# Optimization experiments

Measured on AMD Instinct MI355X. Metric: run time of the kernel, lower is better.

The kernel has to match this reference:

```python
import jax, jax.numpy as jnp
import numpy as np

N, E = 10000, 320000
F_N, F_E, F_G, LATENT, F_OUT = 128, 128, 32, 128, 128


def _make_mlp_params(key, dims):
    # dims: list of layer widths, e.g. [256,128,128,128,256]
    params = []
    for i in range(len(dims) - 1):
        key, k1, k2 = jax.random.split(key, 3)
        lim = 1.0 / np.sqrt(dims[i])
        w = jax.random.uniform(k1, (dims[i], dims[i + 1]), jnp.float32, -lim, lim)
        b = jax.random.uniform(k2, (dims[i + 1],), jnp.float32, -lim, lim)
        params.append((w, b))
    return params, key


def _mlp(h, ws, bs, activate_final):
    n = len(ws)
    for i in range(n):
        h = h @ ws[i] + bs[i]
        if i < n - 1 or activate_final:
            h = jax.nn.relu(h)
    return h


def setup_inputs() -> dict:
    key = jax.random.key(0)
    key, kx, ke, kg, ki = jax.random.split(key, 5)
    x = jax.random.normal(kx, (N, F_N), jnp.float32)
    edge_index = jax.random.randint(ki, (2, E), 0, N, jnp.int64)
    edge_attr = jax.random.normal(ke, (E, F_E), jnp.float32)
    global_attr = jax.random.normal(kg, (1, F_G), jnp.float32)

    # node_mlp_1: (F_N+F_E) -> L -> L -> L -> (F_N+F_E), activate_final=True
    p1, key = _make_mlp_params(key, [F_N + F_E, LATENT, LATENT, LATENT, F_N + F_E])
    # node_mlp_2: (2*F_N+F_E+F_G) -> L -> L -> L -> F_OUT, activate_final=False
    p2, key = _make_mlp_params(key, [2 * F_N + F_E + F_G, LATENT, LATENT, LATENT, F_OUT])

    inp = {"x": x, "edge_index": edge_index, "edge_attr": edge_attr, "global_attr": global_attr}
    for i, (w, b) in enumerate(p1):
        inp[f"m1_w{i}"] = w
        inp[f"m1_b{i}"] = b
    for i, (w, b) in enumerate(p2):
        inp[f"m2_w{i}"] = w
        inp[f"m2_b{i}"] = b
    return inp


def reference(x, edge_index, edge_attr, global_attr,
              m1_w0, m1_b0, m1_w1, m1_b1, m1_w2, m1_b2, m1_w3, m1_b3,
              m2_w0, m2_b0, m2_w1, m2_b1, m2_w2, m2_b2, m2_w3, m2_b3):
    row, col = edge_index[0], edge_index[1]
    n = x.shape[0]
    # gather sender-side node feats, per-edge MLP (activate_final=True)
    h = jnp.concatenate([x[row], edge_attr], axis=1)          # [E, F_N+F_E]
    h = _mlp(h, [m1_w0, m1_w1, m1_w2, m1_w3], [m1_b0, m1_b1, m1_b2, m1_b3], True)
    # scatter_mean over destination nodes
    s = jax.ops.segment_sum(h, col, num_segments=n)           # [N, F_N+F_E]
    cnt = jax.ops.segment_sum(jnp.ones((h.shape[0],), h.dtype), col, num_segments=n)
    agg = s / jnp.maximum(cnt, 1.0)[:, None]
    # repeat global feats to N rows (pad_to_size mode='repeat', G divides N)
    g = jnp.tile(global_attr, (n // global_attr.shape[0], 1))  # [N, F_G]
    out = jnp.concatenate([x, agg, g], axis=1)                 # [N, 2F_N+F_E+F_G]
    return _mlp(out, [m2_w0, m2_w1, m2_w2, m2_w3], [m2_b0, m2_b1, m2_b2, m2_b3], False)
```

## Files before the change

kernel.cpp:

```cpp
#include <hip/hip_runtime.h>

#define E_EDGES 320000
#define N_NODES 10000

typedef __attribute__((ext_vector_type(8))) short short8;
typedef __attribute__((ext_vector_type(4))) float floatx4;
typedef __attribute__((ext_vector_type(4))) short short4v;

__device__ __forceinline__ float bf2f(unsigned short u) {
    union { unsigned int i; float f; } v; v.i = ((unsigned int)u) << 16; return v.f;
}
__device__ __forceinline__ unsigned short f2bf(float f) {
    union { float f; unsigned int i; } v; v.f = f;
    unsigned int u = v.i;
    return (unsigned short)((u + 0x7fffu + ((u >> 16) & 1u)) >> 16);
}

template<int K, int Nn, int NT>
__device__ __forceinline__ void layer_acc(const unsigned short* __restrict__ in, int istride,
                                          const unsigned short* __restrict__ wt,
                                          int lane, int n0, floatx4 (&acc)[4][NT])
{
    const int quad = lane >> 4;
    const int mrow = lane & 15;
    floatx4 zero = {0.f, 0.f, 0.f, 0.f};
#pragma unroll
    for (int mt = 0; mt < 4; ++mt)
#pragma unroll
        for (int nt = 0; nt < NT; ++nt)
            acc[mt][nt] = zero;

#pragma unroll
    for (int kt = 0; kt < K / 32; ++kt) {
        const int koff = kt * 32 + quad * 8;
        short8 a[4];
        short8 b[NT];
#pragma unroll
        for (int mt = 0; mt < 4; ++mt)
            a[mt] = *(const short8*)&in[(mt * 16 + mrow) * istride + koff];
#pragma unroll
        for (int nt = 0; nt < NT; ++nt)
            b[nt] = *(const short8*)&wt[(size_t)(kt * (Nn >> 4) + (n0 >> 4) + nt) * 512 + lane * 8];
#pragma unroll
        for (int nt = 0; nt < NT; ++nt)
#pragma unroll
            for (int mt = 0; mt < 4; ++mt)
                acc[mt][nt] = __builtin_amdgcn_mfma_f32_16x16x32_bf16(a[mt], b[nt], acc[mt][nt], 0, 0, 0);
    }
}

template<int NT>
__device__ __forceinline__ void store_lds(floatx4 (&acc)[4][NT], const float* __restrict__ bias,
                                          int lane, int n0, unsigned short* __restrict__ out, int ostride,
                                          bool relu)
{
    const int quad = lane >> 4, mrow = lane & 15;
#pragma unroll
    for (int nt = 0; nt < NT; ++nt) {
        int col = n0 + nt * 16 + mrow;
        float bv = bias[col];
#pragma unroll
        for (int mt = 0; mt < 4; ++mt) {
#pragma unroll
            for (int r = 0; r < 4; ++r) {
                float v = acc[mt][nt][r] + bv;
                if (relu) v = v > 0.f ? v : 0.f;
                out[(mt * 16 + quad * 4 + r) * ostride + col] = f2bf(v);
            }
        }
    }
}

struct TDesc { const float* src; unsigned short* dst; int nElem; int logN; int blockStart; };
struct TArgs { TDesc d[8]; };

__global__ void transpose_kernel(TArgs a)
{
    int b = blockIdx.x;
    int i = 0;
#pragma unroll
    for (int j = 1; j < 8; ++j)
        if (b >= a.d[j].blockStart) i = j;
    const TDesc t = a.d[i];
    int idx = (b - t.blockStart) * 256 + threadIdx.x;
    if (idx < t.nElem) {
        int n = idx & ((1 << t.logN) - 1);
        int k = idx >> t.logN;
        int ntiles = 1 << (t.logN - 4);
        size_t dsti = ((size_t)(k >> 5) * ntiles + (n >> 4)) * 512
                    + ((k >> 3) & 3) * 128 + (n & 15) * 8 + (k & 7);
        t.dst[dsti] = f2bf(t.src[idx]);
    }
}

__global__ void hist_kernel(const int* __restrict__ eidx, int* __restrict__ cnt)
{
    int e = blockIdx.x * 256 + threadIdx.x;
    atomicAdd(&cnt[eidx[E_EDGES + e]], 1);
}

__global__ void scan_kernel(const int* __restrict__ cnt, int* __restrict__ fill)
{
    __shared__ int partial[256];
    const int CH = 40;
    int tid = threadIdx.x;
    int base = tid * CH;
    int local[CH];
    int sum = 0;
#pragma unroll
    for (int j = 0; j < CH; ++j) {
        int idx = base + j;
        int c = (idx < N_NODES) ? cnt[idx] : 0;
        local[j] = c;
        sum += c;
    }
    partial[tid] = sum;
    __syncthreads();
    for (int o = 1; o < 256; o <<= 1) {
        int v = (tid >= o) ? partial[tid - o] : 0;
        __syncthreads();
        partial[tid] += v;
        __syncthreads();
    }
    int run = partial[tid] - sum;
#pragma unroll
    for (int j = 0; j < CH; ++j) {
        int idx = base + j;
        if (idx < N_NODES) fill[idx] = run;
        run += local[j];
    }
}

__global__ void fill_kernel(const int* __restrict__ eidx, int* __restrict__ fill,
                            int* __restrict__ elist, int* __restrict__ rowp, int* __restrict__ dstp)
{
    int e = blockIdx.x * 256 + threadIdx.x;
    int c = eidx[E_EDGES + e];
    int r = eidx[e];
    int pos = atomicAdd(&fill[c], 1);
    elist[pos] = e;
    rowp[pos] = r;
    dstp[pos] = c;
}

__global__ __launch_bounds__(256, 3) void edge_kernel(
    const float* __restrict__ x,
    const float* __restrict__ ea,
    const int* __restrict__ elist, const int* __restrict__ rowp, const int* __restrict__ dstp,
    const unsigned short* __restrict__ wt0, const float* __restrict__ b0,
    const unsigned short* __restrict__ wt1, const float* __restrict__ b1,
    const unsigned short* __restrict__ wt2, const float* __restrict__ b2,
    const unsigned short* __restrict__ wt3, const float* __restrict__ b3,
    float* __restrict__ s)
{
    __shared__ __align__(16) char U[51200];
    __shared__ int es[64];
    __shared__ int rs[64];
    __shared__ int ds[64];

    unsigned short* H0 = (unsigned short*)U;
    unsigned short* H1 = (unsigned short*)(U + 33792);
    unsigned short* H2 = (unsigned short*)U;
    unsigned short* H3 = H1;
    unsigned short* G  = (unsigned short*)U;

    const int tid = threadIdx.x;
    const int p0 = blockIdx.x * 64;

    if (tid < 64) {
        es[tid] = elist[p0 + tid];
        rs[tid] = rowp[p0 + tid];
        ds[tid] = dstp[p0 + tid];
    }
    __syncthreads();

#pragma unroll
    for (int i = 0; i < 16; ++i) {
        int task = tid + i * 256;
        int row = task >> 6, part = task & 63;
        float4 v;
        if (part < 32) v = *(const float4*)(x + (size_t)rs[row] * 128 + part * 4);
        else           v = *(const float4*)(ea + (size_t)es[row] * 128 + (part - 32) * 4);
        short4v o;
        o[0] = (short)f2bf(v.x); o[1] = (short)f2bf(v.y);
        o[2] = (short)f2bf(v.z); o[3] = (short)f2bf(v.w);
        *(short4v*)&H0[row * 264 + part * 4] = o;
    }
    __syncthreads();

    const int lane = tid & 63;
    const int wave = tid >> 6;

    {
        floatx4 acc[4][2];
        layer_acc<256, 128, 2>(H0, 264, wt0, lane, wave * 32, acc);
        store_lds<2>(acc, b0, lane, wave * 32, H1, 136, true);
    }
    __syncthreads();
    {
        floatx4 acc[4][2];
        layer_acc<128, 128, 2>(H1, 136, wt1, lane, wave * 32, acc);
        store_lds<2>(acc, b1, lane, wave * 32, H2, 136, true);
    }
    __syncthreads();
    {
        floatx4 acc[4][2];
        layer_acc<128, 128, 2>(H2, 136, wt2, lane, wave * 32, acc);
        store_lds<2>(acc, b2, lane, wave * 32, H3, 136, true);
    }
    __syncthreads();
    {
        floatx4 acc[4][4];
        layer_acc<128, 256, 4>(H3, 136, wt3, lane, wave * 64, acc);
        __syncthreads();
        const int quad = lane >> 4, mrow = lane & 15;
#pragma unroll
        for (int nt = 0; nt < 4; ++nt) {
            int colg = wave * 64 + nt * 16 + mrow;
            float bv = b3[colg];
#pragma unroll
            for (int mt = 0; mt < 4; ++mt) {
#pragma unroll
                for (int r = 0; r < 4; ++r) {
                    int row = mt * 16 + quad * 4 + r;
                    float v = acc[mt][nt][r] + bv;
                    v = v > 0.f ? v : 0.f;
                    G[row * 264 + colg] = f2bf(v);
                }
            }
        }
    }
    __syncthreads();

    {
        int col = tid;
        float sum = 0.f;
#pragma unroll 4
        for (int i = 0; i < 64; ++i) {
            sum += bf2f(G[i * 264 + col]);
            if (i == 63 || ds[i + 1] != ds[i]) {
                atomicAdd(&s[(size_t)ds[i] * 256 + col], sum);
                sum = 0.f;
            }
        }
    }
}

__global__ __launch_bounds__(256, 2) void node_kernel(
    const float* __restrict__ x,
    const float* __restrict__ g,
    const float* __restrict__ s,
    const int* __restrict__ cnt,
    const unsigned short* __restrict__ wt0, const float* __restrict__ b0,
    const unsigned short* __restrict__ wt1, const float* __restrict__ b1,
    const unsigned short* __restrict__ wt2, const float* __restrict__ b2,
    const unsigned short* __restrict__ wt3, const float* __restrict__ b3,
    float* __restrict__ out)
{
    __shared__ __align__(16) char NU[71680];
    unsigned short* Abig = (unsigned short*)NU;
    unsigned short* HsA  = (unsigned short*)(NU + 54272);
    unsigned short* HsB  = (unsigned short*)NU;

    const int tid = threadIdx.x;
    const int node0 = blockIdx.x * 64;

#pragma unroll
    for (int i = 0; i < 8; ++i) {
        int task = tid + i * 256;
        int row = task >> 5, part = task & 31;
        int node = node0 + row;
        short4v o = {0, 0, 0, 0};
        if (node < N_NODES) {
            float4 v = *(const float4*)(x + (size_t)node * 128 + part * 4);
            o[0] = (short)f2bf(v.x); o[1] = (short)f2bf(v.y);
            o[2] = (short)f2bf(v.z); o[3] = (short)f2bf(v.w);
        }
        *(short4v*)&Abig[row * 424 + part * 4] = o;
    }
#pragma unroll
    for (int i = 0; i < 16; ++i) {
        int task = tid + i * 256;
        int row = task >> 6, part = task & 63;
        int node = node0 + row;
        short4v o = {0, 0, 0, 0};
        if (node < N_NODES) {
            float c = (float)cnt[node];
            float inv = 1.f / (c > 1.f ? c : 1.f);
            floatx4 v = *(const floatx4*)(s + (size_t)node * 256 + part * 4);
            o[0] = (short)f2bf(v[0] * inv);
            o[1] = (short)f2bf(v[1] * inv);
            o[2] = (short)f2bf(v[2] * inv);
            o[3] = (short)f2bf(v[3] * inv);
        }
        *(short4v*)&Abig[row * 424 + 128 + part * 4] = o;
    }
#pragma unroll
    for (int i = 0; i < 2; ++i) {
        int task = tid + i * 256;
        int row = task >> 3, part = task & 7;
        float4 v = *(const float4*)(g + part * 4);
        short4v o;
        o[0] = (short)f2bf(v.x); o[1] = (short)f2bf(v.y);
        o[2] = (short)f2bf(v.z); o[3] = (short)f2bf(v.w);
        *(short4v*)&Abig[row * 424 + 384 + part * 4] = o;
    }
    __syncthreads();

    const int lane = tid & 63;
    const int wave = tid >> 6;

    {
        floatx4 acc[4][2];
        layer_acc<416, 128, 2>(Abig, 424, wt0, lane, wave * 32, acc);
        store_lds<2>(acc, b0, lane, wave * 32, HsA, 136, true);
    }
    __syncthreads();
    {
        floatx4 acc[4][2];
        layer_acc<128, 128, 2>(HsA, 136, wt1, lane, wave * 32, acc);
        __syncthreads();
        store_lds<2>(acc, b1, lane, wave * 32, HsB, 136, true);
    }
    __syncthreads();
    {
        floatx4 acc[4][2];
        layer_acc<128, 128, 2>(HsB, 136, wt2, lane, wave * 32, acc);
        store_lds<2>(acc, b2, lane, wave * 32, HsA, 136, true);
    }
    __syncthreads();
    {
        floatx4 acc[4][2];
        layer_acc<128, 128, 2>(HsA, 136, wt3, lane, wave * 32, acc);
        const int quad = lane >> 4, mrow = lane & 15;
#pragma unroll
        for (int nt = 0; nt < 2; ++nt) {
            int col = wave * 32 + nt * 16 + mrow;
            float bv = b3[col];
#pragma unroll
            for (int mt = 0; mt < 4; ++mt) {
#pragma unroll
                for (int r = 0; r < 4; ++r) {
                    int row = mt * 16 + quad * 4 + r;
                    int node = node0 + row;
                    if (node < N_NODES)
                        out[(size_t)node * 128 + col] = acc[mt][nt][r] + bv;
                }
            }
        }
    }
}

extern "C" void kernel_launch(void* const* d_in, const int* in_sizes, int n_in,
                              void* d_out, int out_size, void* d_ws, size_t ws_size,
                              hipStream_t stream)
{
    (void)in_sizes; (void)n_in; (void)out_size; (void)ws_size;

    const float* x  = (const float*)d_in[0];
    const int* eidx = (const int*)d_in[1];
    const float* ea = (const float*)d_in[2];
    const float* g  = (const float*)d_in[3];

    const float* w1[4]  = { (const float*)d_in[4],  (const float*)d_in[6],
                            (const float*)d_in[8],  (const float*)d_in[10] };
    const float* bb1[4] = { (const float*)d_in[5],  (const float*)d_in[7],
                            (const float*)d_in[9],  (const float*)d_in[11] };
    const float* w2[4]  = { (const float*)d_in[12], (const float*)d_in[14],
                            (const float*)d_in[16], (const float*)d_in[18] };
    const float* bb2[4] = { (const float*)d_in[13], (const float*)d_in[15],
                            (const float*)d_in[17], (const float*)d_in[19] };

    char* p = (char*)d_ws;
    unsigned short* wt1_0 = (unsigned short*)p; p += 256 * 128 * 2;
    unsigned short* wt1_1 = (unsigned short*)p; p += 128 * 128 * 2;
    unsigned short* wt1_2 = (unsigned short*)p; p += 128 * 128 * 2;
    unsigned short* wt1_3 = (unsigned short*)p; p += 128 * 256 * 2;
    unsigned short* wt2_0 = (unsigned short*)p; p += 416 * 128 * 2;
    unsigned short* wt2_1 = (unsigned short*)p; p += 128 * 128 * 2;
    unsigned short* wt2_2 = (unsigned short*)p; p += 128 * 128 * 2;
    unsigned short* wt2_3 = (unsigned short*)p; p += 128 * 128 * 2;
    float* s   = (float*)p; p += (size_t)N_NODES * 256 * 4;
    int* cnt   = (int*)p;   p += (size_t)N_NODES * 4;
    int* fill  = (int*)p;   p += (size_t)N_NODES * 4;
    int* elist = (int*)p;   p += (size_t)E_EDGES * 4;
    int* rowp  = (int*)p;   p += (size_t)E_EDGES * 4;
    int* dstp  = (int*)p;   p += (size_t)E_EDGES * 4;

    hipMemsetAsync(s, 0, (size_t)N_NODES * 256 * 4 + (size_t)N_NODES * 4, stream);

    TArgs ta;
    int bs = 0;
    auto set = [&](int i, const float* src, unsigned short* dst, int K, int Nn, int logN) {
        ta.d[i].src = src; ta.d[i].dst = dst; ta.d[i].nElem = K * Nn;
        ta.d[i].logN = logN; ta.d[i].blockStart = bs;
        bs += (K * Nn + 255) / 256;
    };
    set(0, w1[0], wt1_0, 256, 128, 7);
    set(1, w1[1], wt1_1, 128, 128, 7);
    set(2, w1[2], wt1_2, 128, 128, 7);
    set(3, w1[3], wt1_3, 128, 256, 8);
    set(4, w2[0], wt2_0, 416, 128, 7);
    set(5, w2[1], wt2_1, 128, 128, 7);
    set(6, w2[2], wt2_2, 128, 128, 7);
    set(7, w2[3], wt2_3, 128, 128, 7);

    hipLaunchKernelGGL(transpose_kernel, dim3(bs), dim3(256), 0, stream, ta);
    hipLaunchKernelGGL(hist_kernel, dim3(E_EDGES / 256), dim3(256), 0, stream, eidx, cnt);
    hipLaunchKernelGGL(scan_kernel, dim3(1), dim3(256), 0, stream, cnt, fill);
    hipLaunchKernelGGL(fill_kernel, dim3(E_EDGES / 256), dim3(256), 0, stream,
                       eidx, fill, elist, rowp, dstp);

    hipLaunchKernelGGL(edge_kernel, dim3(E_EDGES / 64), dim3(256), 0, stream,
                       x, ea, elist, rowp, dstp,
                       wt1_0, bb1[0], wt1_1, bb1[1], wt1_2, bb1[2], wt1_3, bb1[3],
                       s);

    hipLaunchKernelGGL(node_kernel, dim3((N_NODES + 63) / 64), dim3(256), 0, stream,
                       x, g, s, cnt,
                       wt2_0, bb2[0], wt2_1, bb2[1], wt2_2, bb2[2], wt2_3, bb2[3],
                       (float*)d_out);
}
```

Baseline: 494.7 us.

## Swap MFMA operand roles so epilogue writes packed vector stores; fuse hist into prep

```diff
diff --git a/kernel.cpp b/kernel.cpp
--- a/kernel.cpp
+++ b/kernel.cpp
@@ -1,72 +1,77 @@
 #include <hip/hip_runtime.h>
+#include <hip/hip_bf16.h>
 
 #define E_EDGES 320000
 #define N_NODES 10000
 
 typedef __attribute__((ext_vector_type(8))) short short8;
 typedef __attribute__((ext_vector_type(4))) float floatx4;
-typedef __attribute__((ext_vector_type(4))) short short4v;
 
 __device__ __forceinline__ float bf2f(unsigned short u) {
     union { unsigned int i; float f; } v; v.i = ((unsigned int)u) << 16; return v.f;
 }
-__device__ __forceinline__ unsigned short f2bf(float f) {
-    union { float f; unsigned int i; } v; v.f = f;
-    unsigned int u = v.i;
-    return (unsigned short)((u + 0x7fffu + ((u >> 16) & 1u)) >> 16);
-}
-
-template<int K, int Nn, int NT>
+__device__ __forceinline__ unsigned int pk2(float a, float b) {
+    float2 t; t.x = a; t.y = b;
+    __hip_bfloat162 h = __float22bfloat162_rn(t);
+    union { __hip_bfloat162 h; unsigned int u; } c; c.h = h; return c.u;
+}
+
+template<int K, int Nn, int FT, int ET>
 __device__ __forceinline__ void layer_acc(const unsigned short* __restrict__ in, int istride,
                                           const unsigned short* __restrict__ wt,
-                                          int lane, int n0, floatx4 (&acc)[4][NT])
+                                          int lane, int n0, floatx4 (&acc)[FT][ET])
 {
     const int quad = lane >> 4;
     const int mrow = lane & 15;
     floatx4 zero = {0.f, 0.f, 0.f, 0.f};
 #pragma unroll
-    for (int mt = 0; mt < 4; ++mt)
-#pragma unroll
-        for (int nt = 0; nt < NT; ++nt)
-            acc[mt][nt] = zero;
+    for (int ft = 0; ft < FT; ++ft)
+#pragma unroll
+        for (int et = 0; et < ET; ++et)
+            acc[ft][et] = zero;
 
 #pragma unroll
     for (int kt = 0; kt < K / 32; ++kt) {
         const int koff = kt * 32 + quad * 8;
-        short8 a[4];
-        short8 b[NT];
-#pragma unroll
-        for (int mt = 0; mt < 4; ++mt)
-            a[mt] = *(const short8*)&in[(mt * 16 + mrow) * istride + koff];
-#pragma unroll
-        for (int nt = 0; nt < NT; ++nt)
-            b[nt] = *(const short8*)&wt[(size_t)(kt * (Nn >> 4) + (n0 >> 4) + nt) * 512 + lane * 8];
-#pragma unroll
-        for (int nt = 0; nt < NT; ++nt)
-#pragma unroll
-            for (int mt = 0; mt < 4; ++mt)
-                acc[mt][nt] = __builtin_amdgcn_mfma_f32_16x16x32_bf16(a[mt], b[nt], acc[mt][nt], 0, 0, 0);
-    }
-}
-
-template<int NT>
-__device__ __forceinline__ void store_lds(floatx4 (&acc)[4][NT], const float* __restrict__ bias,
+        short8 a[FT];
+        short8 b[ET];
+#pragma unroll
+        for (int ft = 0; ft < FT; ++ft)
+            a[ft] = *(const short8*)&wt[(size_t)(kt * (Nn >> 4) + (n0 >> 4) + ft) * 512 + lane * 8];
+#pragma unroll
+        for (int et = 0; et < ET; ++et)
+            b[et] = *(const short8*)&in[(et * 16 + mrow) * istride + koff];
+#pragma unroll
+        for (int ft = 0; ft < FT; ++ft)
+#pragma unroll
+            for (int et = 0; et < ET; ++et)
+                acc[ft][et] = __builtin_amdgcn_mfma_f32_16x16x32_bf16(a[ft], b[et], acc[ft][et], 0, 0, 0);
+    }
+}
+
+template<int FT, int ET>
+__device__ __forceinline__ void store_lds(floatx4 (&acc)[FT][ET], const float* __restrict__ bias,
                                           int lane, int n0, unsigned short* __restrict__ out, int ostride,
                                           bool relu)
 {
     const int quad = lane >> 4, mrow = lane & 15;
 #pragma unroll
-    for (int nt = 0; nt < NT; ++nt) {
-        int col = n0 + nt * 16 + mrow;
-        float bv = bias[col];
-#pragma unroll
-        for (int mt = 0; mt < 4; ++mt) {
-#pragma unroll
-            for (int r = 0; r < 4; ++r) {
-                float v = acc[mt][nt][r] + bv;
-                if (relu) v = v > 0.f ? v : 0.f;
-                out[(mt * 16 + quad * 4 + r) * ostride + col] = f2bf(v);
+    for (int ft = 0; ft < FT; ++ft) {
+        int fbase = n0 + ft * 16 + quad * 4;
+        float4 bv = *(const float4*)&bias[fbase];
+#pragma unroll
+        for (int et = 0; et < ET; ++et) {
+            int edge = et * 16 + mrow;
+            float v0 = acc[ft][et][0] + bv.x;
+            float v1 = acc[ft][et][1] + bv.y;
+            float v2 = acc[ft][et][2] + bv.z;
+            float v3 = acc[ft][et][3] + bv.w;
+            if (relu) {
+                v0 = v0 > 0.f ? v0 : 0.f; v1 = v1 > 0.f ? v1 : 0.f;
+                v2 = v2 > 0.f ? v2 : 0.f; v3 = v3 > 0.f ? v3 : 0.f;
             }
+            uint2 pk; pk.x = pk2(v0, v1); pk.y = pk2(v2, v3);
+            *(uint2*)&out[edge * ostride + fbase] = pk;
         }
     }
 }
@@ -74,9 +79,14 @@
 struct TDesc { const float* src; unsigned short* dst; int nElem; int logN; int blockStart; };
 struct TArgs { TDesc d[8]; };
 
-__global__ void transpose_kernel(TArgs a)
+__global__ void prep_kernel(TArgs a, const int* __restrict__ eidx, int* __restrict__ cnt, int histStart)
 {
     int b = blockIdx.x;
+    if (b >= histStart) {
+        int e = (b - histStart) * 256 + threadIdx.x;
+        if (e < E_EDGES) atomicAdd(&cnt[eidx[E_EDGES + e]], 1);
+        return;
+    }
     int i = 0;
 #pragma unroll
     for (int j = 1; j < 8; ++j)
@@ -89,14 +99,10 @@
         int ntiles = 1 << (t.logN - 4);
         size_t dsti = ((size_t)(k >> 5) * ntiles + (n >> 4)) * 512
                     + ((k >> 3) & 3) * 128 + (n & 15) * 8 + (k & 7);
-        t.dst[dsti] = f2bf(t.src[idx]);
-    }
-}
-
-__global__ void hist_kernel(const int* __restrict__ eidx, int* __restrict__ cnt)
-{
-    int e = blockIdx.x * 256 + threadIdx.x;
-    atomicAdd(&cnt[eidx[E_EDGES + e]], 1);
+        union { float f; unsigned int u; } c; c.f = t.src[idx];
+        unsigned int uu = c.u;
+        t.dst[dsti] = (unsigned short)((uu + 0x7fffu + ((uu >> 16) & 1u)) >> 16);
+    }
 }
 
 __global__ void scan_kernel(const int* __restrict__ cnt, int* __restrict__ fill)
@@ -181,10 +187,8 @@
         float4 v;
         if (part < 32) v = *(const float4*)(x + (size_t)rs[row] * 128 + part * 4);
         else           v = *(const float4*)(ea + (size_t)es[row] * 128 + (part - 32) * 4);
-        short4v o;
-        o[0] = (short)f2bf(v.x); o[1] = (short)f2bf(v.y);
-        o[2] = (short)f2bf(v.z); o[3] = (short)f2bf(v.w);
-        *(short4v*)&H0[row * 264 + part * 4] = o;
+        uint2 pk; pk.x = pk2(v.x, v.y); pk.y = pk2(v.z, v.w);
+        *(uint2*)&H0[row * 264 + part * 4] = pk;
     }
     __syncthreads();
 
@@ -192,55 +196,47 @@
     const int wave = tid >> 6;
 
     {
-        floatx4 acc[4][2];
-        layer_acc<256, 128, 2>(H0, 264, wt0, lane, wave * 32, acc);
-        store_lds<2>(acc, b0, lane, wave * 32, H1, 136, true);
-    }
-    __syncthreads();
-    {
-        floatx4 acc[4][2];
-        layer_acc<128, 128, 2>(H1, 136, wt1, lane, wave * 32, acc);
-        store_lds<2>(acc, b1, lane, wave * 32, H2, 136, true);
-    }
-    __syncthreads();
-    {
-        floatx4 acc[4][2];
-        layer_acc<128, 128, 2>(H2, 136, wt2, lane, wave * 32, acc);
-        store_lds<2>(acc, b2, lane, wave * 32, H3, 136, true);
+        floatx4 acc[2][4];
+        layer_acc<256, 128, 2, 4>(H0, 264, wt0, lane, wave * 32, acc);
+        store_lds<2, 4>(acc, b0, lane, wave * 32, H1, 136, true);
+    }
+    __syncthreads();
+    {
+        floatx4 acc[2][4];
+        layer_acc<128, 128, 2, 4>(H1, 136, wt1, lane, wave * 32, acc);
+        store_lds<2, 4>(acc, b1, lane, wave * 32, H2, 136, true);
+    }
+    __syncthreads();
+    {
+        floatx4 acc[2][4];
+        layer_acc<128, 128, 2, 4>(H2, 136, wt2, lane, wave * 32, acc);
+        store_lds<2, 4>(acc, b2, lane, wave * 32, H3, 136, true);
     }
     __syncthreads();
     {
         floatx4 acc[4][4];
-        layer_acc<128, 256, 4>(H3, 136, wt3, lane, wave * 64, acc);
-        __syncthreads();
-        const int quad = lane >> 4, mrow = lane & 15;
-#pragma unroll
-        for (int nt = 0; nt < 4; ++nt) {
-            int colg = wave * 64 + nt * 16 + mrow;
-            float bv = b3[colg];
-#pragma unroll
-            for (int mt = 0; mt < 4; ++mt) {
-#pragma unroll
-                for (int r = 0; r < 4; ++r) {
-                    int row = mt * 16 + quad * 4 + r;
-                    float v = acc[mt][nt][r] + bv;
-                    v = v > 0.f ? v : 0.f;
-                    G[row * 264 + colg] = f2bf(v);
-                }
-            }
-        }
-    }
-    __syncthreads();
-
-    {
-        int col = tid;
-        float sum = 0.f;
+        layer_acc<128, 256, 4, 4>(H3, 136, wt3, lane, wave * 64, acc);
+        store_lds<4, 4>(acc, b3, lane, wave * 64, G, 264, true);
+    }
+    __syncthreads();
+
+    {
+        int p = tid & 127;
+        int half = tid >> 7;
+        int col2 = p * 2;
+        int base = half * 32;
+        float s0 = 0.f, s1 = 0.f;
 #pragma unroll 4
-        for (int i = 0; i < 64; ++i) {
-            sum += bf2f(G[i * 264 + col]);
-            if (i == 63 || ds[i + 1] != ds[i]) {
-                atomicAdd(&s[(size_t)ds[i] * 256 + col], sum);
-                sum = 0.f;
+        for (int i = 0; i < 32; ++i) {
+            int gi = base + i;
+            unsigned int u = *(const unsigned int*)&G[gi * 264 + col2];
+            s0 += bf2f((unsigned short)u);
+            s1 += bf2f((unsigned short)(u >> 16));
+            if (i == 31 || ds[gi + 1] != ds[gi]) {
+                float* dst = &s[(size_t)ds[gi] * 256 + col2];
+                atomicAdd(dst, s0);
+                atomicAdd(dst + 1, s1);
+                s0 = 0.f; s1 = 0.f;
             }
         }
     }
@@ -270,40 +266,35 @@
         int task = tid + i * 256;
         int row = task >> 5, part = task & 31;
         int node = node0 + row;
-        short4v o = {0, 0, 0, 0};
+        uint2 pk = {0u, 0u};
         if (node < N_NODES) {
             float4 v = *(const float4*)(x + (size_t)node * 128 + part * 4);
-            o[0] = (short)f2bf(v.x); o[1] = (short)f2bf(v.y);
-            o[2] = (short)f2bf(v.z); o[3] = (short)f2bf(v.w);
+            pk.x = pk2(v.x, v.y); pk.y = pk2(v.z, v.w);
         }
-        *(short4v*)&Abig[row * 424 + part * 4] = o;
+        *(uint2*)&Abig[row * 424 + part * 4] = pk;
     }
 #pragma unroll
     for (int i = 0; i < 16; ++i) {
         int task = tid + i * 256;
         int row = task >> 6, part = task & 63;
         int node = node0 + row;
-        short4v o = {0, 0, 0, 0};
+        uint2 pk = {0u, 0u};
         if (node < N_NODES) {
             float c = (float)cnt[node];
             float inv = 1.f / (c > 1.f ? c : 1.f);
             floatx4 v = *(const floatx4*)(s + (size_t)node * 256 + part * 4);
-            o[0] = (short)f2bf(v[0] * inv);
-            o[1] = (short)f2bf(v[1] * inv);
-            o[2] = (short)f2bf(v[2] * inv);
-            o[3] = (short)f2bf(v[3] * inv);
+            pk.x = pk2(v[0] * inv, v[1] * inv);
+            pk.y = pk2(v[2] * inv, v[3] * inv);
         }
-        *(short4v*)&Abig[row * 424 + 128 + part * 4] = o;
+        *(uint2*)&Abig[row * 424 + 128 + part * 4] = pk;
     }
 #pragma unroll
     for (int i = 0; i < 2; ++i) {
         int task = tid + i * 256;
         int row = task >> 3, part = task & 7;
         float4 v = *(const float4*)(g + part * 4);
-        short4v o;
-        o[0] = (short)f2bf(v.x); o[1] = (short)f2bf(v.y);
-        o[2] = (short)f2bf(v.z); o[3] = (short)f2bf(v.w);
-        *(short4v*)&Abig[row * 424 + 384 + part * 4] = o;
+        uint2 pk; pk.x = pk2(v.x, v.y); pk.y = pk2(v.z, v.w);
+        *(uint2*)&Abig[row * 424 + 384 + part * 4] = pk;
     }
     __syncthreads();
 
@@ -311,40 +302,41 @@
     const int wave = tid >> 6;
 
     {
-        floatx4 acc[4][2];
-        layer_acc<416, 128, 2>(Abig, 424, wt0, lane, wave * 32, acc);
-        store_lds<2>(acc, b0, lane, wave * 32, HsA, 136, true);
-    }
-    __syncthreads();
-    {
-        floatx4 acc[4][2];
-        layer_acc<128, 128, 2>(HsA, 136, wt1, lane, wave * 32, acc);
-        __syncthreads();
-        store_lds<2>(acc, b1, lane, wave * 32, HsB, 136, true);
-    }
-    __syncthreads();
-    {
-        floatx4 acc[4][2];
-        layer_acc<128, 128, 2>(HsB, 136, wt2, lane, wave * 32, acc);
-        store_lds<2>(acc, b2, lane, wave * 32, HsA, 136, true);
-    }
-    __syncthreads();
-    {
-        floatx4 acc[4][2];
-        layer_acc<128, 128, 2>(HsA, 136, wt3, lane, wave * 32, acc);
+        floatx4 acc[2][4];
+        layer_acc<416, 128, 2, 4>(Abig, 424, wt0, lane, wave * 32, acc);
+        store_lds<2, 4>(acc, b0, lane, wave * 32, HsA, 136, true);
+    }
+    __syncthreads();
+    {
+        floatx4 acc[2][4];
+        layer_acc<128, 128, 2, 4>(HsA, 136, wt1, lane, wave * 32, acc);
+        store_lds<2, 4>(acc, b1, lane, wave * 32, HsB, 136, true);
+    }
+    __syncthreads();
+    {
+        floatx4 acc[2][4];
+        layer_acc<128, 128, 2, 4>(HsB, 136, wt2, lane, wave * 32, acc);
+        store_lds<2, 4>(acc, b2, lane, wave * 32, HsA, 136, true);
+    }
+    __syncthreads();
+    {
+        floatx4 acc[2][4];
+        layer_acc<128, 128, 2, 4>(HsA, 136, wt3, lane, wave * 32, acc);
         const int quad = lane >> 4, mrow = lane & 15;
 #pragma unroll
-        for (int nt = 0; nt < 2; ++nt) {
-            int col = wave * 32 + nt * 16 + mrow;
-            float bv = b3[col];
-#pragma unroll
-            for (int mt = 0; mt < 4; ++mt) {
-#pragma unroll
-                for (int r = 0; r < 4; ++r) {
-                    int row = mt * 16 + quad * 4 + r;
-                    int node = node0 + row;
-                    if (node < N_NODES)
-                        out[(size_t)node * 128 + col] = acc[mt][nt][r] + bv;
+        for (int ft = 0; ft < 2; ++ft) {
+            int fbase = wave * 32 + ft * 16 + quad * 4;
+            float4 bv = *(const float4*)&b3[fbase];
+#pragma unroll
+            for (int et = 0; et < 4; ++et) {
+                int node = node0 + et * 16 + mrow;
+                if (node < N_NODES) {
+                    float4 o;
+                    o.x = acc[ft][et][0] + bv.x;
+                    o.y = acc[ft][et][1] + bv.y;
+                    o.z = acc[ft][et][2] + bv.z;
+                    o.w = acc[ft][et][3] + bv.w;
+                    *(float4*)&out[(size_t)node * 128 + fbase] = o;
                 }
             }
         }
@@ -405,8 +397,9 @@
     set(6, w2[2], wt2_2, 128, 128, 7);
     set(7, w2[3], wt2_3, 128, 128, 7);
 
-    hipLaunchKernelGGL(transpose_kernel, dim3(bs), dim3(256), 0, stream, ta);
-    hipLaunchKernelGGL(hist_kernel, dim3(E_EDGES / 256), dim3(256), 0, stream, eidx, cnt);
+    int histBlocks = E_EDGES / 256;
+    hipLaunchKernelGGL(prep_kernel, dim3(bs + histBlocks), dim3(256), 0, stream,
+                       ta, eidx, cnt, bs);
     hipLaunchKernelGGL(scan_kernel, dim3(1), dim3(256), 0, stream, cnt, fill);
     hipLaunchKernelGGL(fill_kernel, dim3(E_EDGES / 256), dim3(256), 0, stream,
                        eidx, fill, elist, rowp, dstp);
```

Measured after the change: 475.6 us. -3.9%, faster.
